# Performance work log

Hardware: AMD Instinct MI355X
Metric: run time of the kernel (lower is better)

Reference implementation:

```python
import jax, jax.numpy as jnp
import numpy as np

B, L, E, D = 32, 1024, 512, 512  # batch, seq_len, input_size, per-direction hidden
SCALE = 1.4142135623730951  # rescale=True, highway_bias=0 -> sqrt(1+exp(0*2)) = sqrt(2)


def setup_inputs() -> dict:
    key = jax.random.key(0)
    ks = jax.random.split(key, 12)
    g = lambda k, shape, s: (jax.random.normal(k, shape, jnp.float32) * s)
    return {
        "seqs": jax.random.normal(ks[0], (B, L, E), jnp.float32),
        # layer 0: input E -> 2 dirs * 4 projections * D
        "W0": g(ks[1], (E, 8 * D), (1.0 / E) ** 0.5),
        "vf0": g(ks[2], (2, D), 0.1), "vr0": g(ks[3], (2, D), 0.1),
        "bf0": jnp.zeros((2, D), jnp.float32), "br0": jnp.zeros((2, D), jnp.float32),
        # layer 1: input 2D -> 2 dirs * 4 projections * D
        "W1": g(ks[4], (2 * D, 8 * D), (1.0 / (2 * D)) ** 0.5),
        "vf1": g(ks[5], (2, D), 0.1), "vr1": g(ks[6], (2, D), 0.1),
        "bf1": jnp.zeros((2, D), jnp.float32), "br1": jnp.zeros((2, D), jnp.float32),
        "lengths": jax.random.randint(ks[7], (B,), 1, L + 1, dtype=jnp.int32),
    }


def _sru_dir(u, vf, vr, bf, br, reverse):
    # u: (L, B, 4, D) -> h: (L, B, D), c_T: (B, D)
    def step(c, u_t):
        xt, fp, rp, xp = u_t[:, 0], u_t[:, 1], u_t[:, 2], u_t[:, 3]
        f = jax.nn.sigmoid(fp + vf * c + bf)
        c_new = f * c + (1.0 - f) * xt
        r = jax.nn.sigmoid(rp + vr * c + br)
        h = r * c_new + (1.0 - r) * xp * SCALE
        return c_new, h

    c0 = jnp.zeros((u.shape[1], u.shape[-1]), u.dtype)
    cT, hs = jax.lax.scan(step, c0, u, reverse=reverse)
    return hs, cT


def _sru_layer(x, W, vf, vr, bf, br):
    # x: (L, B, n_in)
    Lx, Bx = x.shape[0], x.shape[1]
    U = (x @ W).reshape(Lx, Bx, 2, 4, -1)  # dirs, (x_tilde, f, r, x_resid)
    h_f, c_f = _sru_dir(U[:, :, 0], vf[0], vr[0], bf[0], br[0], False)
    h_b, c_b = _sru_dir(U[:, :, 1], vf[1], vr[1], bf[1], br[1], True)
    return jnp.concatenate([h_f, h_b], -1), jnp.concatenate([c_f, c_b], -1)


def reference(seqs, W0, vf0, vr0, bf0, br0, W1, vf1, vr1, bf1, br1, lengths):
    x = jnp.transpose(seqs, (1, 0, 2))  # (L, B, E)
    out0, _ = _sru_layer(x, W0, vf0, vr0, bf0, br0)
    out1, c1 = _sru_layer(out0, W1, vf1, vr1, bf1, br1)
    # module returns (h[1], output.transpose(0,1)): layer-1 final cell state, (B,L,2D) outputs
    return c1, jnp.transpose(out1, (1, 0, 2))
```

## Files before the change

kernel.cpp:

```cpp
#include <hip/hip_runtime.h>
#include <cstdint>
#include <cstddef>

#define B_   32
#define L_   1024
#define D_   512
#define M_   (B_ * L_)
#define N8D  4096
#define SCALEF 1.4142135623730951f
#define LOG2E 1.4426950408889634f

typedef unsigned short u16;
typedef __bf16 bf16x8 __attribute__((ext_vector_type(8)));
typedef unsigned short u16x8 __attribute__((ext_vector_type(8)));
typedef unsigned short u16x4 __attribute__((ext_vector_type(4)));
typedef float f32x4 __attribute__((ext_vector_type(4)));

__device__ __forceinline__ float bf2f(u16 u) {
    union { unsigned int i; float f; } v; v.i = ((unsigned int)u) << 16; return v.f;
}
__device__ __forceinline__ u16 f2bf(float x) {
    union { float f; unsigned int i; } v; v.f = x;
    unsigned int r = (v.i + 0x7fffu + ((v.i >> 16) & 1u)) >> 16;
    return (u16)r;
}
__device__ __forceinline__ float sigmoid_fast(float z) {
    return __builtin_amdgcn_rcpf(1.0f + __builtin_amdgcn_exp2f(-LOG2E * z));
}

__device__ __forceinline__ void gl2lds16(const u16* g, u16* l) {
    __builtin_amdgcn_global_load_lds(
        (const __attribute__((address_space(1))) void*)g,
        (__attribute__((address_space(3))) void*)l, 16, 0, 0);
}

#define VMW(n) asm volatile("s_waitcnt vmcnt(" #n ")" ::: "memory")
#define LGK(n) asm volatile("s_waitcnt lgkmcnt(" #n ")" ::: "memory")
#define SB     __builtin_amdgcn_sched_barrier(0)

__global__ __launch_bounds__(256) void f32_to_bf16(const float* __restrict__ in,
                                                   u16* __restrict__ out) {
    size_t i = ((size_t)blockIdx.x * 256 + threadIdx.x) * 8;
    f32x4 v0 = *(const f32x4*)(in + i);
    f32x4 v1 = *(const f32x4*)(in + i + 4);
    u16x8 o;
#pragma unroll
    for (int q = 0; q < 4; ++q) { o[q] = f2bf(v0[q]); o[4 + q] = f2bf(v1[q]); }
    *(u16x8*)(out + i) = o;
}

__global__ __launch_bounds__(256) void transpose_w(const float* __restrict__ in,
                                                   u16* __restrict__ out,
                                                   int R, int C) {
    __shared__ u16 tile[32][33];
    int bx = blockIdx.x * 32;
    int by = blockIdx.y * 32;
    int tx = threadIdx.x & 31;
    int ty = threadIdx.x >> 5;
#pragma unroll
    for (int i = 0; i < 32; i += 8)
        tile[ty + i][tx] = f2bf(in[(size_t)(by + ty + i) * C + bx + tx]);
    __syncthreads();
#pragma unroll
    for (int i = 0; i < 32; i += 8) {
        int n = bx + ty + i;
        int p = (n >> 11) * 2048 + ((n & 511) << 2) + ((n >> 9) & 3);
        out[(size_t)p * R + by + tx] = tile[tx][ty + i];
    }
}

__global__ __launch_bounds__(256, 2) void gemm128(const u16* __restrict__ A,
                                                  const u16* __restrict__ BT,
                                                  u16* __restrict__ U, int K) {
    extern __shared__ __align__(16) u16 lds[];
    const int t    = threadIdx.x;
    const int lane = t & 63;
    const int wn   = t >> 6;
    const int qm   = lane & 15;
    const int quad = lane >> 4;

    const int nwg = gridDim.x;
    const int wg  = blockIdx.x;
    const int swz = (wg & 7) * (nwg >> 3) + (wg >> 3);
    const int bn  = (swz & 15) << 8;
    const int bm  = (swz >> 4) << 7;

    const int P0   = t * 16;
    const int L0   = P0 ^ ((P0 >> 3) & 0x30);
    const int srow = L0 >> 6;
    const int scol = (L0 & 63) >> 1;
    const u16* Ag = A  + (size_t)(bm + srow) * K + scol;
    const u16* Bg = BT + (size_t)(bn + srow) * K + scol;
    const size_t g64 = (size_t)64 * K;
    u16* ldst = lds + t * 8;

    const int fxor = (quad * 16) ^ ((qm & 6) << 3);
    const int aL   = qm * 64 + fxor;
    const int bL   = (wn * 64 + qm) * 64 + fxor;
    const char* ldsc = (const char*)lds;

    f32x4 acc[8][4];
#pragma unroll
    for (int i = 0; i < 8; ++i)
#pragma unroll
        for (int j = 0; j < 4; ++j) acc[i][j] = (f32x4)(0.0f);

#define RD16(p) (*(const bf16x8*)(p))

#define STG6(kt, bb) do {                                                    \
        const u16* a_ = Ag + (size_t)(kt) * 32;                              \
        const u16* b_ = Bg + (size_t)(kt) * 32;                              \
        u16* la = ldst + (bb) / 2;                                           \
        gl2lds16(a_,       la);                                              \
        gl2lds16(a_ + g64, la + 2048);                                       \
        u16* lb = ldst + (bb) / 2 + 4096;                                    \
        gl2lds16(b_,           lb);                                          \
        gl2lds16(b_ + g64,     lb + 2048);                                   \
        gl2lds16(b_ + 2 * g64, lb + 4096);                                   \
        gl2lds16(b_ + 3 * g64, lb + 6144);                                   \
    } while (0)

#define G4(g, av) do {                                                       \
        _Pragma("unroll")                                                    \
        for (int nj = 0; nj < 4; ++nj)                                       \
            acc[g][nj] = __builtin_amdgcn_mfma_f32_16x16x32_bf16(            \
                av, bbf[nj], acc[g][nj], 0, 0, 0);                           \
    } while (0)

#define PH(bb, STAGE_STMT, VM_STMT) do {                                     \
        const char* As_ = ldsc + (bb);                                       \
        const char* Bs_ = ldsc + (bb) + 8192;                                \
        bf16x8 bbf[4], aa[8];                                                \
        bbf[0] = RD16(Bs_ + bL);        SB;                                  \
        bbf[1] = RD16(Bs_ + bL + 1024); SB;                                  \
        bbf[2] = RD16(Bs_ + bL + 2048); SB;                                  \
        bbf[3] = RD16(Bs_ + bL + 3072); SB;                                  \
        aa[0] = RD16(As_ + aL);        SB;                                   \
        aa[1] = RD16(As_ + aL + 1024); SB;                                   \
        aa[2] = RD16(As_ + aL + 2048); SB;                                   \
        aa[3] = RD16(As_ + aL + 3072); SB;                                   \
        aa[4] = RD16(As_ + aL + 4096); SB;                                   \
        aa[5] = RD16(As_ + aL + 5120); SB;                                   \
        aa[6] = RD16(As_ + aL + 6144); SB;                                   \
        aa[7] = RD16(As_ + aL + 7168); SB;                                   \
        STAGE_STMT;                                                          \
        __builtin_amdgcn_s_setprio(1);                                       \
        LGK(7); SB; G4(0, aa[0]); SB;                                        \
        LGK(6); SB; G4(1, aa[1]); SB;                                        \
        LGK(5); SB; G4(2, aa[2]); SB;                                        \
        LGK(4); SB; G4(3, aa[3]); SB;                                        \
        LGK(3); SB; G4(4, aa[4]); SB;                                        \
        LGK(2); SB; G4(5, aa[5]); SB;                                        \
        LGK(1); SB; G4(6, aa[6]); SB;                                        \
        LGK(0); SB; G4(7, aa[7]); SB;                                        \
        __builtin_amdgcn_s_setprio(0);                                       \
        VM_STMT;                                                             \
        SB; __builtin_amdgcn_s_barrier(); SB;                                \
    } while (0)

    const int nt = K >> 5;

    STG6(0, 0); STG6(1, 24576);
    VMW(6);
    __builtin_amdgcn_s_barrier();

    int bb = 0, bs = 49152;
    for (int tt = 0; tt + 2 < nt; ++tt) {
        PH(bb, STG6(tt + 2, bs), VMW(6));
        bb += 24576; if (bb == 73728) bb = 0;
        bs += 24576; if (bs == 73728) bs = 0;
    }
    PH(bb, , VMW(0));
    bb += 24576; if (bb == 73728) bb = 0;
    PH(bb, , );

#undef PH
#undef G4
#undef STG6
#undef RD16

#pragma unroll
    for (int i8 = 0; i8 < 8; ++i8) {
        const int row0 = bm + i8 * 16 + quad * 4;
#pragma unroll
        for (int nj = 0; nj < 4; ++nj) {
            const int col = bn + wn * 64 + nj * 16 + qm;
#pragma unroll
            for (int r = 0; r < 4; ++r)
                U[(size_t)(row0 + r) * N8D + col] = f2bf(acc[i8][nj][r]);
        }
    }
}

template<bool OUT_F32>
__global__ __launch_bounds__(64) void sru_scan(const u16* __restrict__ U,
                                               const float* __restrict__ vf,
                                               const float* __restrict__ vr,
                                               const float* __restrict__ bfv,
                                               const float* __restrict__ brv,
                                               void* __restrict__ Hv,
                                               void* __restrict__ Cv) {
    constexpr int PF = 32;
    constexpr int NB = L_ / PF;

    int gid = blockIdx.x * blockDim.x + threadIdx.x;
    int d   = gid & (D_ - 1);
    int dir = (gid >> 9) & 1;
    int b   = gid >> 10;
    int ch  = dir * D_ + d;

    const float vf_v = vf[ch];
    const float vr_v = vr[ch];
    const float bf_v = bfv[ch];
    const float br_v = brv[ch];

    const ptrdiff_t ustep = dir ? -(ptrdiff_t)N8D : (ptrdiff_t)N8D;
    const ptrdiff_t hstep = dir ? -(ptrdiff_t)1024 : (ptrdiff_t)1024;
    const u16* p0 = U + (size_t)b * L_ * N8D + dir * 2048 + d * 4
                      + (dir ? (size_t)(L_ - 1) * N8D : 0);
    const size_t hstart = (size_t)b * L_ * 1024 + ch + (dir ? (size_t)(L_ - 1) * 1024 : 0);
    float* Hf = (float*)Hv + hstart;
    u16*   Hh = (u16*)Hv + hstart;

    float c = 0.0f;

    auto loadB = [&](u16x4 (&buf)[PF], int tb) {
        const u16* base = p0 + (ptrdiff_t)tb * PF * ustep;
#pragma unroll
        for (int i = 0; i < PF; ++i)
            buf[i] = *(const u16x4*)(base + (ptrdiff_t)i * ustep);
    };
    auto compStore = [&](u16x4 (&buf)[PF], int tb) {
        const ptrdiff_t hb = (ptrdiff_t)tb * PF * hstep;
#pragma unroll
        for (int i = 0; i < PF; ++i) {
            float xt = bf2f(buf[i][0]), fp = bf2f(buf[i][1]);
            float rp = bf2f(buf[i][2]), xp = bf2f(buf[i][3]);
            float f = sigmoid_fast(fp + vf_v * c + bf_v);
            float r = sigmoid_fast(rp + vr_v * c + br_v);
            c = f * (c - xt) + xt;
            float xs = xp * SCALEF;
            float h  = r * (c - xs) + xs;
            ptrdiff_t ho = hb + (ptrdiff_t)i * hstep;
            if (OUT_F32) Hf[ho] = h; else Hh[ho] = f2bf(h);
        }
    };

    u16x4 b0[PF], b1[PF];
    loadB(b0, 0);
    loadB(b1, 1);
    for (int t = 0; t < NB; t += 2) {
        compStore(b0, t);
        if (t + 2 < NB) loadB(b0, t + 2);
        compStore(b1, t + 1);
        if (t + 3 < NB) loadB(b1, t + 3);
    }

    if (OUT_F32) ((float*)Cv)[b * 1024 + ch] = c;
    else         ((u16*)Cv)[b * 1024 + ch]  = f2bf(c);
}

extern "C" void kernel_launch(void* const* d_in, const int* in_sizes, int n_in,
                              void* d_out, int out_size, void* d_ws, size_t ws_size,
                              hipStream_t stream) {
    (void)in_sizes; (void)n_in; (void)out_size; (void)ws_size;

    const float* seqs = (const float*)d_in[0];
    const float* W0   = (const float*)d_in[1];
    const float* vf0  = (const float*)d_in[2];
    const float* vr0  = (const float*)d_in[3];
    const float* bf0  = (const float*)d_in[4];
    const float* br0  = (const float*)d_in[5];
    const float* W1   = (const float*)d_in[6];
    const float* vf1  = (const float*)d_in[7];
    const float* vr1  = (const float*)d_in[8];
    const float* bf1  = (const float*)d_in[9];
    const float* br1  = (const float*)d_in[10];

    float* out = (float*)d_out;
    char* ws = (char*)d_ws;

    const size_t U_BYTES  = (size_t)M_ * N8D * 2;
    const size_t H_BYTES  = (size_t)M_ * 1024 * 2;
    const size_t W0T_B    = (size_t)4096 * 512 * 2;
    const size_t W1T_B    = (size_t)4096 * 1024 * 2;

    u16* U   = (u16*)(ws);
    u16* H0  = (u16*)(ws + U_BYTES);
    u16* S16 = H0;
    u16* W0T = (u16*)(ws + U_BYTES + H_BYTES);
    u16* W1T = (u16*)(ws + U_BYTES + H_BYTES + W0T_B);
    u16* Cd  = (u16*)(ws + U_BYTES + H_BYTES + W0T_B + W1T_B);

    f32_to_bf16<<<dim3(M_ * 512 / 8 / 256), 256, 0, stream>>>(seqs, S16);

    transpose_w<<<dim3(4096 / 32, 512 / 32), 256, 0, stream>>>(W0, W0T, 512, 4096);
    transpose_w<<<dim3(4096 / 32, 1024 / 32), 256, 0, stream>>>(W1, W1T, 1024, 4096);

    gemm128<<<dim3(4096), 256, 73728, stream>>>(S16, W0T, U, 512);
    sru_scan<false><<<dim3(512), 64, 0, stream>>>(U, vf0, vr0, bf0, br0, (void*)H0, (void*)Cd);

    gemm128<<<dim3(4096), 256, 73728, stream>>>(H0, W1T, U, 1024);
    sru_scan<true><<<dim3(512), 64, 0, stream>>>(U, vf1, vr1, bf1, br1,
                                                 (void*)(out + B_ * 1024), (void*)out);
}
```

Before: 807.5 us.

## Load GEMM A operand directly to registers and stage only B in LDS

The GEMM kernel now loads the A operand tile straight from global memory into registers, double-buffered across iterations, and stages only B through a 4-slot LDS ring. The wave layout changes from 1x4 (each wave 128x64) to 2x2 (each wave 64x128), so each wave reads 8 B fragments from LDS and holds 4 A fragments in registers. This is meant to cut LDS traffic and footprint (64KB static instead of 72KB dynamic) and overlap global A loads with MFMA. In exchange it uses more registers and relies on uncoalesced 16-byte direct global loads for A.

```diff
diff --git a/kernel.cpp b/kernel.cpp
--- a/kernel.cpp
+++ b/kernel.cpp
@@ -69,13 +69,15 @@
     }
 }
 
-__global__ __launch_bounds__(256, 2) void gemm128(const u16* __restrict__ A,
-                                                  const u16* __restrict__ BT,
-                                                  u16* __restrict__ U, int K) {
-    extern __shared__ __align__(16) u16 lds[];
+__global__ __launch_bounds__(256, 2) void gemm_hyb(const u16* __restrict__ A,
+                                                   const u16* __restrict__ BT,
+                                                   u16* __restrict__ U, int K) {
+    __shared__ __align__(16) u16 ldsB[4 * 8192];
     const int t    = threadIdx.x;
     const int lane = t & 63;
-    const int wn   = t >> 6;
+    const int wave = t >> 6;
+    const int mi   = wave >> 1;
+    const int ni   = wave & 1;
     const int qm   = lane & 15;
     const int quad = lane >> 4;
 
@@ -89,105 +91,104 @@
     const int L0   = P0 ^ ((P0 >> 3) & 0x30);
     const int srow = L0 >> 6;
     const int scol = (L0 & 63) >> 1;
-    const u16* Ag = A  + (size_t)(bm + srow) * K + scol;
     const u16* Bg = BT + (size_t)(bn + srow) * K + scol;
     const size_t g64 = (size_t)64 * K;
-    u16* ldst = lds + t * 8;
+    u16* ldst = ldsB + t * 8;
 
     const int fxor = (quad * 16) ^ ((qm & 6) << 3);
-    const int aL   = qm * 64 + fxor;
-    const int bL   = (wn * 64 + qm) * 64 + fxor;
-    const char* ldsc = (const char*)lds;
-
-    f32x4 acc[8][4];
-#pragma unroll
-    for (int i = 0; i < 8; ++i)
-#pragma unroll
-        for (int j = 0; j < 4; ++j) acc[i][j] = (f32x4)(0.0f);
+    const int bL   = (ni * 128 + qm) * 64 + fxor;
+    const char* ldsc = (const char*)ldsB;
+
+    const u16* pA = A + (size_t)(bm + mi * 64 + qm) * K + quad * 8;
+    const size_t aM = (size_t)16 * K;
+
+    f32x4 acc[4][8];
+#pragma unroll
+    for (int i = 0; i < 4; ++i)
+#pragma unroll
+        for (int j = 0; j < 8; ++j) acc[i][j] = (f32x4)(0.0f);
+
+    bf16x8 a0[4], a1[4];
 
 #define RD16(p) (*(const bf16x8*)(p))
 
-#define STG6(kt, bb) do {                                                    \
-        const u16* a_ = Ag + (size_t)(kt) * 32;                              \
+#define LDA(dst, kt) do {                                                    \
+        const u16* a_ = pA + (size_t)(kt) * 32;                              \
+        dst[0] = RD16(a_);          dst[1] = RD16(a_ + aM);                  \
+        dst[2] = RD16(a_ + 2 * aM); dst[3] = RD16(a_ + 3 * aM);              \
+    } while (0)
+
+#define STGB(kt, slot) do {                                                  \
         const u16* b_ = Bg + (size_t)(kt) * 32;                              \
-        u16* la = ldst + (bb) / 2;                                           \
-        gl2lds16(a_,       la);                                              \
-        gl2lds16(a_ + g64, la + 2048);                                       \
-        u16* lb = ldst + (bb) / 2 + 4096;                                    \
+        u16* lb = ldst + (slot) * 8192;                                      \
         gl2lds16(b_,           lb);                                          \
         gl2lds16(b_ + g64,     lb + 2048);                                   \
         gl2lds16(b_ + 2 * g64, lb + 4096);                                   \
         gl2lds16(b_ + 3 * g64, lb + 6144);                                   \
     } while (0)
 
-#define G4(g, av) do {                                                       \
+#define GN(j, aC) do {                                                       \
         _Pragma("unroll")                                                    \
-        for (int nj = 0; nj < 4; ++nj)                                       \
-            acc[g][nj] = __builtin_amdgcn_mfma_f32_16x16x32_bf16(            \
-                av, bbf[nj], acc[g][nj], 0, 0, 0);                           \
+        for (int mj = 0; mj < 4; ++mj)                                       \
+            acc[mj][j] = __builtin_amdgcn_mfma_f32_16x16x32_bf16(            \
+                aC[mj], bbf[j], acc[mj][j], 0, 0, 0);                        \
     } while (0)
 
-#define PH(bb, STAGE_STMT, VM_STMT) do {                                     \
-        const char* As_ = ldsc + (bb);                                       \
-        const char* Bs_ = ldsc + (bb) + 8192;                                \
-        bf16x8 bbf[4], aa[8];                                                \
+#define PHASE(tt, aC, aN, DO_A, DO_B, VMN) do {                              \
+        if (DO_A) { LDA(aN, (tt) + 1); } SB;                                 \
+        if (DO_B) { STGB((tt) + 2, ((tt) + 2) & 3); } SB;                    \
+        VMW(VMN);                                                            \
+        __builtin_amdgcn_s_barrier();                                        \
+        const char* Bs_ = ldsc + (((tt) & 3) * 16384);                       \
+        bf16x8 bbf[8];                                                       \
         bbf[0] = RD16(Bs_ + bL);        SB;                                  \
         bbf[1] = RD16(Bs_ + bL + 1024); SB;                                  \
         bbf[2] = RD16(Bs_ + bL + 2048); SB;                                  \
         bbf[3] = RD16(Bs_ + bL + 3072); SB;                                  \
-        aa[0] = RD16(As_ + aL);        SB;                                   \
-        aa[1] = RD16(As_ + aL + 1024); SB;                                   \
-        aa[2] = RD16(As_ + aL + 2048); SB;                                   \
-        aa[3] = RD16(As_ + aL + 3072); SB;                                   \
-        aa[4] = RD16(As_ + aL + 4096); SB;                                   \
-        aa[5] = RD16(As_ + aL + 5120); SB;                                   \
-        aa[6] = RD16(As_ + aL + 6144); SB;                                   \
-        aa[7] = RD16(As_ + aL + 7168); SB;                                   \
-        STAGE_STMT;                                                          \
+        bbf[4] = RD16(Bs_ + bL + 4096); SB;                                  \
+        bbf[5] = RD16(Bs_ + bL + 5120); SB;                                  \
+        bbf[6] = RD16(Bs_ + bL + 6144); SB;                                  \
+        bbf[7] = RD16(Bs_ + bL + 7168); SB;                                  \
         __builtin_amdgcn_s_setprio(1);                                       \
-        LGK(7); SB; G4(0, aa[0]); SB;                                        \
-        LGK(6); SB; G4(1, aa[1]); SB;                                        \
-        LGK(5); SB; G4(2, aa[2]); SB;                                        \
-        LGK(4); SB; G4(3, aa[3]); SB;                                        \
-        LGK(3); SB; G4(4, aa[4]); SB;                                        \
-        LGK(2); SB; G4(5, aa[5]); SB;                                        \
-        LGK(1); SB; G4(6, aa[6]); SB;                                        \
-        LGK(0); SB; G4(7, aa[7]); SB;                                        \
+        LGK(7); SB; GN(0, aC); SB;                                           \
+        LGK(6); SB; GN(1, aC); SB;                                           \
+        LGK(5); SB; GN(2, aC); SB;                                           \
+        LGK(4); SB; GN(3, aC); SB;                                           \
+        LGK(3); SB; GN(4, aC); SB;                                           \
+        LGK(2); SB; GN(5, aC); SB;                                           \
+        LGK(1); SB; GN(6, aC); SB;                                           \
+        LGK(0); SB; GN(7, aC); SB;                                           \
         __builtin_amdgcn_s_setprio(0);                                       \
-        VM_STMT;                                                             \
-        SB; __builtin_amdgcn_s_barrier(); SB;                                \
     } while (0)
 
     const int nt = K >> 5;
 
-    STG6(0, 0); STG6(1, 24576);
-    VMW(6);
-    __builtin_amdgcn_s_barrier();
-
-    int bb = 0, bs = 49152;
-    for (int tt = 0; tt + 2 < nt; ++tt) {
-        PH(bb, STG6(tt + 2, bs), VMW(6));
-        bb += 24576; if (bb == 73728) bb = 0;
-        bs += 24576; if (bs == 73728) bs = 0;
+    LDA(a0, 0); SB;
+    STGB(0, 0); STGB(1, 1); SB;
+    VMW(4);
+
+    for (int tt = 0; tt < nt - 2; tt += 2) {
+        PHASE(tt,     a0, a1, 1, 1, 12);
+        PHASE(tt + 1, a1, a0, 1, 1, 12);
     }
-    PH(bb, , VMW(0));
-    bb += 24576; if (bb == 73728) bb = 0;
-    PH(bb, , );
-
-#undef PH
-#undef G4
-#undef STG6
+    PHASE(nt - 2, a0, a1, 1, 0, 8);
+    PHASE(nt - 1, a1, a0, 0, 0, 0);
+
+#undef PHASE
+#undef GN
+#undef STGB
+#undef LDA
 #undef RD16
 
 #pragma unroll
-    for (int i8 = 0; i8 < 8; ++i8) {
-        const int row0 = bm + i8 * 16 + quad * 4;
-#pragma unroll
-        for (int nj = 0; nj < 4; ++nj) {
-            const int col = bn + wn * 64 + nj * 16 + qm;
+    for (int mj = 0; mj < 4; ++mj) {
+        const int row0 = bm + mi * 64 + mj * 16 + quad * 4;
+#pragma unroll
+        for (int nj = 0; nj < 8; ++nj) {
+            const int col = bn + ni * 128 + nj * 16 + qm;
 #pragma unroll
             for (int r = 0; r < 4; ++r)
-                U[(size_t)(row0 + r) * N8D + col] = f2bf(acc[i8][nj][r]);
+                U[(size_t)(row0 + r) * N8D + col] = f2bf(acc[mj][nj][r]);
         }
     }
 }
@@ -297,10 +298,10 @@
     transpose_w<<<dim3(4096 / 32, 512 / 32), 256, 0, stream>>>(W0, W0T, 512, 4096);
     transpose_w<<<dim3(4096 / 32, 1024 / 32), 256, 0, stream>>>(W1, W1T, 1024, 4096);
 
-    gemm128<<<dim3(4096), 256, 73728, stream>>>(S16, W0T, U, 512);
+    gemm_hyb<<<dim3(4096), 256, 0, stream>>>(S16, W0T, U, 512);
     sru_scan<false><<<dim3(512), 64, 0, stream>>>(U, vf0, vr0, bf0, br0, (void*)H0, (void*)Cd);
 
-    gemm128<<<dim3(4096), 256, 73728, stream>>>(H0, W1T, U, 1024);
+    gemm_hyb<<<dim3(4096), 256, 0, stream>>>(H0, W1T, U, 1024);
     sru_scan<true><<<dim3(512), 64, 0, stream>>>(U, vf1, vr1, bf1, br1,
                                                  (void*)(out + B_ * 1024), (void*)out);
 }
```

After: 956.4 us. 1.18x slower.
